# Optimization experiments

Hardware: AMD Instinct MI355X
Metric: run time of the kernel (lower is better)

Reference implementation:

```python
import jax, jax.numpy as jnp
import numpy as np

QUERY_DIM = 1024
KV_DIM = 768
NUM_HEADS = 16
HEAD_DIM = QUERY_DIM // NUM_HEADS


def setup_inputs() -> dict:
    key = jax.random.key(0)
    ks = jax.random.split(key, 11)
    B, Sq, Skv = 4, 2048, 2048
    s_q = 1.0 / np.sqrt(QUERY_DIM)
    s_kv = 1.0 / np.sqrt(KV_DIM)
    return {
        "query": jax.random.normal(ks[0], (B, Sq, QUERY_DIM), jnp.float32),
        "key": jax.random.normal(ks[1], (B, Skv, KV_DIM), jnp.float32),
        "value": jax.random.normal(ks[2], (B, Skv, KV_DIM), jnp.float32),
        "Wq": jax.random.uniform(ks[3], (QUERY_DIM, QUERY_DIM), jnp.float32, -s_q, s_q),
        "bq": jax.random.uniform(ks[4], (QUERY_DIM,), jnp.float32, -s_q, s_q),
        "Wk": jax.random.uniform(ks[5], (KV_DIM, QUERY_DIM), jnp.float32, -s_kv, s_kv),
        "bk": jax.random.uniform(ks[6], (QUERY_DIM,), jnp.float32, -s_kv, s_kv),
        "Wv": jax.random.uniform(ks[7], (KV_DIM, QUERY_DIM), jnp.float32, -s_kv, s_kv),
        "bv": jax.random.uniform(ks[8], (QUERY_DIM,), jnp.float32, -s_kv, s_kv),
        "Wo": jax.random.uniform(ks[9], (QUERY_DIM, QUERY_DIM), jnp.float32, -s_q, s_q),
        "bo": jax.random.uniform(ks[10], (QUERY_DIM,), jnp.float32, -s_q, s_q),
    }


def reference(query, key, value, Wq, bq, Wk, bk, Wv, bv, Wo, bo):
    B, Sq, _ = query.shape
    Skv = key.shape[1]
    H, D = NUM_HEADS, HEAD_DIM
    # linear projections, then split heads: [B, H, S, D]
    q = (query @ Wq + bq).reshape(B, Sq, H, D).transpose(0, 2, 1, 3)
    k = (key @ Wk + bk).reshape(B, Skv, H, D).transpose(0, 2, 1, 3)
    v = (value @ Wv + bv).reshape(B, Skv, H, D).transpose(0, 2, 1, 3)
    scores = jnp.einsum("bhqd,bhkd->bhqk", q, k) / np.sqrt(D).astype(jnp.float32)
    probs = jax.nn.softmax(scores, axis=-1)
    ctx = jnp.einsum("bhqk,bhkd->bhqd", probs, v)
    ctx = ctx.transpose(0, 2, 1, 3).reshape(B, Sq, H * D)
    return ctx @ Wo + bo
```

## Files before the change

### kernel.cpp

```cpp
#include <hip/hip_runtime.h>

typedef unsigned short u16;
typedef unsigned int u32;
typedef __attribute__((ext_vector_type(8))) short bf16x8;
typedef __attribute__((ext_vector_type(4))) float f32x4;

__device__ __forceinline__ u16 f2bf(float f) {
  union { float f; u32 u; } v; v.f = f;
  u32 r = v.u + 0x7fffu + ((v.u >> 16) & 1u);
  return (u16)(r >> 16);
}
__device__ __forceinline__ u16 f2bf_fast(float f) {
  union { float f; u32 u; } v; v.f = f;
  return (u16)((v.u + 0x8000u) >> 16);
}

__device__ __forceinline__ void gll16(const u16* g, u16* l) {
  __builtin_amdgcn_global_load_lds((__attribute__((address_space(1))) void*)(void*)g,
                                   (__attribute__((address_space(3))) void*)(void*)l,
                                   16, 0, 0);
}

__global__ void conv_bf16(const float* __restrict__ in, u16* __restrict__ out, int n) {
  int i = (blockIdx.x * 256 + threadIdx.x) * 4;
  if (i < n) {
    float4 v = *(const float4*)(in + i);
    ushort4 o;
    o.x = f2bf(v.x); o.y = f2bf(v.y); o.z = f2bf(v.z); o.w = f2bf(v.w);
    *(ushort4*)(out + i) = o;
  }
}

__global__ void transpose_bf16(const float* __restrict__ W, u16* __restrict__ T,
                               int K, int N) {
  __shared__ u16 tile[64 * 72];
  const int k0 = blockIdx.x * 64, n0 = blockIdx.y * 64;
  const int t = threadIdx.x, c = t & 63, rb = t >> 6;
#pragma unroll
  for (int rr = 0; rr < 64; rr += 4) {
    int r = rr + rb;
    tile[r * 72 + c] = f2bf(W[(size_t)(k0 + r) * N + n0 + c]);
  }
  __syncthreads();
#pragma unroll
  for (int rr = 0; rr < 64; rr += 4) {
    int n = rr + rb;
    T[(size_t)(n0 + n) * K + k0 + c] = tile[c * 72 + n];
  }
}

__global__ __launch_bounds__(256, 3) void gemm_bf16(
    const u16* __restrict__ A, const u16* __restrict__ Bt,
    const float* __restrict__ bias, u16* __restrict__ outb,
    float* __restrict__ outf, int K, int mode) {
  __shared__ __align__(16) u16 smem[18432];
  u16* lA = smem;
  u16* lB = smem + 128 * 64;
  const int tid = threadIdx.x;
  const int bm = blockIdx.x * 128;
  const int bn = blockIdx.y * 128;
  const int wid = tid >> 6, lane = tid & 63;
  const int wm = (wid >> 1) * 64, wn = (wid & 1) * 64;
  const int lrow = lane & 15, quad = lane >> 4;
  const int wrow = lane >> 3, wchk = lane & 7;
  const int sw = lrow & 7;
  f32x4 acc[4][4] = {};
  for (int k0 = 0; k0 < K; k0 += 64) {
    const u16* gA = A + (size_t)(bm + wid * 32) * K + k0;
    const u16* gB = Bt + (size_t)(bn + wid * 32) * K + k0;
#pragma unroll
    for (int c = 0; c < 4; c++) {
      gll16(gA + (size_t)(c * 8 + wrow) * K + (wchk ^ wrow) * 8, &lA[(wid * 32 + c * 8) * 64]);
      gll16(gB + (size_t)(c * 8 + wrow) * K + (wchk ^ wrow) * 8, &lB[(wid * 32 + c * 8) * 64]);
    }
    __syncthreads();
#pragma unroll
    for (int ks = 0; ks < 2; ks++) {
      bf16x8 af[4], bfr[4];
#pragma unroll
      for (int i = 0; i < 4; i++)
        af[i] = *(const bf16x8*)&lA[(wm + i * 16 + lrow) * 64 + ((ks * 4 + quad) ^ sw) * 8];
#pragma unroll
      for (int j = 0; j < 4; j++)
        bfr[j] = *(const bf16x8*)&lB[(wn + j * 16 + lrow) * 64 + ((ks * 4 + quad) ^ sw) * 8];
#pragma unroll
      for (int i = 0; i < 4; i++)
#pragma unroll
        for (int j = 0; j < 4; j++)
          acc[i][j] = __builtin_amdgcn_mfma_f32_16x16x32_bf16(af[i], bfr[j], acc[i][j], 0, 0, 0);
    }
    __syncthreads();
  }
  if (mode == 1) {
    u16* tile = smem + wid * (64 * 72);
#pragma unroll
    for (int i = 0; i < 4; i++)
#pragma unroll
      for (int j = 0; j < 4; j++)
#pragma unroll
        for (int r = 0; r < 4; r++) {
          int s_l = i * 16 + quad * 4 + r;
          int d_l = j * 16 + lrow;
          tile[d_l * 72 + s_l] = f2bf(acc[i][j][r] + bias[bn + wn + d_l]);
        }
    __syncthreads();
#pragma unroll
    for (int dd = 0; dd < 8; dd++) {
      int d_l = dd * 8 + (lane >> 3);
      int s_l = (lane & 7) * 8;
      bf16x8 vv = *(const bf16x8*)&tile[d_l * 72 + s_l];
      int row = bm + wm + s_l;
      int col = bn + wn + d_l;
      int b = row >> 11, s = row & 2047;
      int h = col >> 6, d = col & 63;
      *(bf16x8*)&outb[((size_t)(b * 16 + h) * 64 + d) * 2048 + s] = vv;
    }
    return;
  }
#pragma unroll
  for (int i = 0; i < 4; i++)
#pragma unroll
    for (int j = 0; j < 4; j++)
#pragma unroll
      for (int r = 0; r < 4; r++) {
        int row = bm + wm + i * 16 + quad * 4 + r;
        int col = bn + wn + j * 16 + lrow;
        float v = acc[i][j][r] + bias[col];
        if (mode == 2) {
          outf[(size_t)row * 1024 + col] = v;
        } else {
          int b = row >> 11, s = row & 2047;
          int h = col >> 6, d = col & 63;
          outb[((size_t)(b * 16 + h) * 2048 + s) * 64 + d] = f2bf(v);
        }
      }
}

__global__ __launch_bounds__(256, 3) void flash_attn(
    const u16* __restrict__ Q, const u16* __restrict__ Kt,
    const u16* __restrict__ Vt, u16* __restrict__ ctx) {
  __shared__ __align__(16) u16 lK[128 * 64];
  __shared__ __align__(16) u16 lV[64 * 128];
  __shared__ __align__(16) u16 lP[4][16 * 136];
  const int bh = blockIdx.x;
  const int q0 = blockIdx.y * 64;
  const int tid = threadIdx.x, wid = tid >> 6, lane = tid & 63;
  const int lrow = lane & 15, quad = lane >> 4;
  const int sw = lrow & 7;
  const size_t base = (size_t)bh * 2048 * 64;
  bf16x8 qf[2];
#pragma unroll
  for (int ks = 0; ks < 2; ks++)
    qf[ks] = *(const bf16x8*)(Q + base + (size_t)(q0 + wid * 16 + lrow) * 64 + ks * 32 + quad * 8);
  f32x4 of[4] = {};
  float lsum[4] = {0.f, 0.f, 0.f, 0.f};
  const int wrow8 = lane >> 3, wchk8 = lane & 7;
  const int wrow16 = lane >> 4, wchk16 = lane & 15;
  const float C = 0.18033688011112042f;
  for (int kv0 = 0; kv0 < 2048; kv0 += 128) {
    __syncthreads();
    const u16* gK = Kt + base + (size_t)(kv0 + wid * 32) * 64;
    const u16* gV = Vt + base + (size_t)(wid * 16) * 2048 + kv0;
#pragma unroll
    for (int c = 0; c < 4; c++) {
      gll16(gK + (size_t)(c * 8 + wrow8) * 64 + (wchk8 ^ wrow8) * 8,
            &lK[(wid * 32 + c * 8) * 64]);
      gll16(gV + (size_t)(c * 4 + wrow16) * 2048 + (wchk16 ^ (c * 4 + wrow16)) * 8,
            &lV[(wid * 16 + c * 4) * 128]);
    }
    __syncthreads();
    f32x4 sf[8];
#pragma unroll
    for (int n = 0; n < 8; n++) {
      bf16x8 k0f = *(const bf16x8*)&lK[(n * 16 + lrow) * 64 + (quad ^ sw) * 8];
      bf16x8 k1f = *(const bf16x8*)&lK[(n * 16 + lrow) * 64 + ((4 + quad) ^ sw) * 8];
      f32x4 s = {};
      s = __builtin_amdgcn_mfma_f32_16x16x32_bf16(qf[0], k0f, s, 0, 0, 0);
      s = __builtin_amdgcn_mfma_f32_16x16x32_bf16(qf[1], k1f, s, 0, 0, 0);
      sf[n] = s;
    }
#pragma unroll
    for (int n = 0; n < 8; n++)
#pragma unroll
      for (int r = 0; r < 4; r++) {
        float p = __builtin_amdgcn_exp2f(sf[n][r] * C);
        lsum[r] += p;
        lP[wid][(quad * 4 + r) * 136 + n * 16 + lrow] = f2bf_fast(p);
      }
    __syncthreads();
#pragma unroll
    for (int kstep = 0; kstep < 4; kstep++) {
      bf16x8 pf = *(const bf16x8*)&lP[wid][lrow * 136 + kstep * 32 + quad * 8];
#pragma unroll
      for (int n = 0; n < 4; n++) {
        bf16x8 vf = *(const bf16x8*)&lV[(n * 16 + lrow) * 128 + ((kstep * 4 + quad) ^ lrow) * 8];
        of[n] = __builtin_amdgcn_mfma_f32_16x16x32_bf16(pf, vf, of[n], 0, 0, 0);
      }
    }
  }
#pragma unroll
  for (int r = 0; r < 4; r++) {
#pragma unroll
    for (int off = 1; off < 16; off <<= 1) lsum[r] += __shfl_xor(lsum[r], off, 64);
  }
  const int b = bh >> 4, h = bh & 15;
#pragma unroll
  for (int r = 0; r < 4; r++) {
    float inv = 1.f / lsum[r];
#pragma unroll
    for (int n = 0; n < 4; n++) {
      int row = q0 + wid * 16 + quad * 4 + r;
      int col = h * 64 + n * 16 + lrow;
      ctx[((size_t)b * 2048 + row) * 1024 + col] = f2bf(of[n][r] * inv);
    }
  }
}

extern "C" void kernel_launch(void* const* d_in, const int* in_sizes, int n_in,
                              void* d_out, int out_size, void* d_ws, size_t ws_size,
                              hipStream_t stream) {
  const float* query = (const float*)d_in[0];
  const float* key   = (const float*)d_in[1];
  const float* value = (const float*)d_in[2];
  const float* Wq = (const float*)d_in[3];
  const float* bq = (const float*)d_in[4];
  const float* Wk = (const float*)d_in[5];
  const float* bk = (const float*)d_in[6];
  const float* Wv = (const float*)d_in[7];
  const float* bv = (const float*)d_in[8];
  const float* Wo = (const float*)d_in[9];
  const float* bo = (const float*)d_in[10];
  float* out = (float*)d_out;
  char* ws = (char*)d_ws;

  const size_t SZ_QKV = (size_t)8192 * 1024 * 2;
  const size_t SZ_KIN = (size_t)8192 * 768 * 2;
  u16* q_ws  = (u16*)(ws);
  u16* k_ws  = (u16*)(ws + SZ_QKV);
  u16* vt_ws = (u16*)(ws + 2 * SZ_QKV);
  u16* qin   = (u16*)(ws + 3 * SZ_QKV);
  u16* kin   = (u16*)(ws + 4 * SZ_QKV);
  u16* vin   = (u16*)(ws + 4 * SZ_QKV + SZ_KIN);
  u16* ctx   = qin;
  u16* wq_t  = (u16*)(ws + 4 * SZ_QKV + 2 * SZ_KIN);
  u16* wk_t  = wq_t + 1024 * 1024;
  u16* wv_t  = wk_t + 1024 * 768;
  u16* wo_t  = wv_t + 1024 * 768;

  conv_bf16<<<8192, 256, 0, stream>>>(query, qin, 8388608);
  conv_bf16<<<6144, 256, 0, stream>>>(key, kin, 6291456);
  conv_bf16<<<6144, 256, 0, stream>>>(value, vin, 6291456);
  transpose_bf16<<<dim3(16, 16), 256, 0, stream>>>(Wq, wq_t, 1024, 1024);
  transpose_bf16<<<dim3(12, 16), 256, 0, stream>>>(Wk, wk_t, 768, 1024);
  transpose_bf16<<<dim3(12, 16), 256, 0, stream>>>(Wv, wv_t, 768, 1024);
  transpose_bf16<<<dim3(16, 16), 256, 0, stream>>>(Wo, wo_t, 1024, 1024);

  gemm_bf16<<<dim3(64, 8), 256, 0, stream>>>(qin, wq_t, bq, q_ws, nullptr, 1024, 0);
  gemm_bf16<<<dim3(64, 8), 256, 0, stream>>>(kin, wk_t, bk, k_ws, nullptr, 768, 0);
  gemm_bf16<<<dim3(64, 8), 256, 0, stream>>>(vin, wv_t, bv, vt_ws, nullptr, 768, 1);

  flash_attn<<<dim3(64, 32), 256, 0, stream>>>(q_ws, k_ws, vt_ws, ctx);

  gemm_bf16<<<dim3(64, 8), 256, 0, stream>>>(ctx, wo_t, bo, nullptr, out, 1024, 2);
}
```

Baseline: 363.6 us.

## Split flash attention KV tile across waves instead of query rows

Each wave now computes scores for all 64 query rows against its own 32-key slice of the 128-key tile, using transposed MFMAs (K as the A operand). P values are packed two per word, written to a per-wave LDS buffer and read back with only an lgkmcnt wait instead of a block barrier. Partial outputs and row sums are reduced across waves through LDS at the end, with vectorized bf16 stores. The intent is to cut redundant K/V LDS reads and the mid-loop barrier, at the cost of 4x more accumulator registers (64 floats of output per lane), which may hurt occupancy under launch_bounds(256,3), plus a serialized final reduction.

```diff
diff --git a/kernel.cpp b/kernel.cpp
--- a/kernel.cpp
+++ b/kernel.cpp
@@ -2,6 +2,7 @@
 
 typedef unsigned short u16;
 typedef unsigned int u32;
+typedef unsigned long long u64;
 typedef __attribute__((ext_vector_type(8))) short bf16x8;
 typedef __attribute__((ext_vector_type(4))) float f32x4;
 
@@ -10,9 +11,9 @@
   u32 r = v.u + 0x7fffu + ((v.u >> 16) & 1u);
   return (u16)(r >> 16);
 }
-__device__ __forceinline__ u16 f2bf_fast(float f) {
-  union { float f; u32 u; } v; v.f = f;
-  return (u16)((v.u + 0x8000u) >> 16);
+__device__ __forceinline__ u32 pack2bf(float a, float b) {
+  union { float f; u32 u; } x, y; x.f = a; y.f = b;
+  return ((y.u + 0x8000u) & 0xffff0000u) | ((x.u + 0x8000u) >> 16);
 }
 
 __device__ __forceinline__ void gll16(const u16* g, u16* l) {
@@ -139,21 +140,24 @@
 __global__ __launch_bounds__(256, 3) void flash_attn(
     const u16* __restrict__ Q, const u16* __restrict__ Kt,
     const u16* __restrict__ Vt, u16* __restrict__ ctx) {
-  __shared__ __align__(16) u16 lK[128 * 64];
-  __shared__ __align__(16) u16 lV[64 * 128];
-  __shared__ __align__(16) u16 lP[4][16 * 136];
+  __shared__ __align__(16) u16 smem[26624];
+  u16* lK = smem;
+  u16* lV = smem + 8192;
+  const int tid = threadIdx.x, wid = tid >> 6, lane = tid & 63;
+  u16* lP = smem + 16384 + wid * 2560;
   const int bh = blockIdx.x;
   const int q0 = blockIdx.y * 64;
-  const int tid = threadIdx.x, wid = tid >> 6, lane = tid & 63;
   const int lrow = lane & 15, quad = lane >> 4;
   const int sw = lrow & 7;
   const size_t base = (size_t)bh * 2048 * 64;
-  bf16x8 qf[2];
-#pragma unroll
-  for (int ks = 0; ks < 2; ks++)
-    qf[ks] = *(const bf16x8*)(Q + base + (size_t)(q0 + wid * 16 + lrow) * 64 + ks * 32 + quad * 8);
-  f32x4 of[4] = {};
-  float lsum[4] = {0.f, 0.f, 0.f, 0.f};
+  bf16x8 qf[4][2];
+#pragma unroll
+  for (int qt = 0; qt < 4; qt++)
+#pragma unroll
+    for (int ks = 0; ks < 2; ks++)
+      qf[qt][ks] = *(const bf16x8*)(Q + base + (size_t)(q0 + qt * 16 + lrow) * 64 + ks * 32 + quad * 8);
+  f32x4 of[4][4] = {};
+  float lsumq[4] = {0.f, 0.f, 0.f, 0.f};
   const int wrow8 = lane >> 3, wchk8 = lane & 7;
   const int wrow16 = lane >> 4, wchk16 = lane & 15;
   const float C = 0.18033688011112042f;
@@ -169,50 +173,83 @@
             &lV[(wid * 16 + c * 4) * 128]);
     }
     __syncthreads();
-    f32x4 sf[8];
-#pragma unroll
-    for (int n = 0; n < 8; n++) {
-      bf16x8 k0f = *(const bf16x8*)&lK[(n * 16 + lrow) * 64 + (quad ^ sw) * 8];
-      bf16x8 k1f = *(const bf16x8*)&lK[(n * 16 + lrow) * 64 + ((4 + quad) ^ sw) * 8];
-      f32x4 s = {};
-      s = __builtin_amdgcn_mfma_f32_16x16x32_bf16(qf[0], k0f, s, 0, 0, 0);
-      s = __builtin_amdgcn_mfma_f32_16x16x32_bf16(qf[1], k1f, s, 0, 0, 0);
-      sf[n] = s;
-    }
-#pragma unroll
-    for (int n = 0; n < 8; n++)
-#pragma unroll
-      for (int r = 0; r < 4; r++) {
-        float p = __builtin_amdgcn_exp2f(sf[n][r] * C);
-        lsum[r] += p;
-        lP[wid][(quad * 4 + r) * 136 + n * 16 + lrow] = f2bf_fast(p);
+    f32x4 sfT[2][4];
+#pragma unroll
+    for (int nt = 0; nt < 2; nt++) {
+      bf16x8 kf0 = *(const bf16x8*)&lK[((wid * 2 + nt) * 16 + lrow) * 64 + (quad ^ sw) * 8];
+      bf16x8 kf1 = *(const bf16x8*)&lK[((wid * 2 + nt) * 16 + lrow) * 64 + ((4 + quad) ^ sw) * 8];
+#pragma unroll
+      for (int qt = 0; qt < 4; qt++) {
+        f32x4 s = {};
+        s = __builtin_amdgcn_mfma_f32_16x16x32_bf16(kf0, qf[qt][0], s, 0, 0, 0);
+        s = __builtin_amdgcn_mfma_f32_16x16x32_bf16(kf1, qf[qt][1], s, 0, 0, 0);
+        sfT[nt][qt] = s;
       }
-    __syncthreads();
-#pragma unroll
-    for (int kstep = 0; kstep < 4; kstep++) {
-      bf16x8 pf = *(const bf16x8*)&lP[wid][lrow * 136 + kstep * 32 + quad * 8];
-#pragma unroll
-      for (int n = 0; n < 4; n++) {
-        bf16x8 vf = *(const bf16x8*)&lV[(n * 16 + lrow) * 128 + ((kstep * 4 + quad) ^ lrow) * 8];
-        of[n] = __builtin_amdgcn_mfma_f32_16x16x32_bf16(pf, vf, of[n], 0, 0, 0);
+    }
+#pragma unroll
+    for (int nt = 0; nt < 2; nt++)
+#pragma unroll
+      for (int qt = 0; qt < 4; qt++) {
+        float p0 = __builtin_amdgcn_exp2f(sfT[nt][qt][0] * C);
+        float p1 = __builtin_amdgcn_exp2f(sfT[nt][qt][1] * C);
+        float p2 = __builtin_amdgcn_exp2f(sfT[nt][qt][2] * C);
+        float p3 = __builtin_amdgcn_exp2f(sfT[nt][qt][3] * C);
+        lsumq[qt] += (p0 + p1) + (p2 + p3);
+        u64 pk = ((u64)pack2bf(p2, p3) << 32) | pack2bf(p0, p1);
+        *(u64*)&lP[(qt * 16 + lrow) * 40 + nt * 16 + quad * 4] = pk;
       }
-    }
-  }
-#pragma unroll
-  for (int r = 0; r < 4; r++) {
-#pragma unroll
-    for (int off = 1; off < 16; off <<= 1) lsum[r] += __shfl_xor(lsum[r], off, 64);
+    __asm__ volatile("s_waitcnt lgkmcnt(0)" ::: "memory");
+#pragma unroll
+    for (int qt = 0; qt < 4; qt++) {
+      bf16x8 pf = *(const bf16x8*)&lP[(qt * 16 + lrow) * 40 + quad * 8];
+#pragma unroll
+      for (int dt = 0; dt < 4; dt++) {
+        bf16x8 vf = *(const bf16x8*)&lV[(dt * 16 + lrow) * 128 + ((wid * 4 + quad) ^ lrow) * 8];
+        of[qt][dt] = __builtin_amdgcn_mfma_f32_16x16x32_bf16(pf, vf, of[qt][dt], 0, 0, 0);
+      }
+    }
+  }
+  float lsw[4];
+#pragma unroll
+  for (int qt = 0; qt < 4; qt++) {
+    float v = lsumq[qt];
+    v += __shfl_xor(v, 16, 64);
+    v += __shfl_xor(v, 32, 64);
+    lsw[qt] = v;
+  }
+  __syncthreads();
+  float* lsums = (float*)(smem + 16384);
+  if (quad == 0) {
+#pragma unroll
+    for (int qt = 0; qt < 4; qt++) lsums[wid * 64 + qt * 16 + lrow] = lsw[qt];
+  }
+  float* rbuf = (float*)smem;
+  for (int w = 0; w < 4; w++) {
+    if (wid == w) {
+#pragma unroll
+      for (int qt = 0; qt < 4; qt++)
+#pragma unroll
+        for (int dt = 0; dt < 4; dt++)
+#pragma unroll
+          for (int r = 0; r < 4; r++) {
+            int q = qt * 16 + quad * 4 + r;
+            int d = dt * 16 + lrow;
+            if (w == 0) rbuf[q * 66 + d] = of[qt][dt][r];
+            else        rbuf[q * 66 + d] += of[qt][dt][r];
+          }
+    }
+    __syncthreads();
   }
   const int b = bh >> 4, h = bh & 15;
 #pragma unroll
-  for (int r = 0; r < 4; r++) {
-    float inv = 1.f / lsum[r];
-#pragma unroll
-    for (int n = 0; n < 4; n++) {
-      int row = q0 + wid * 16 + quad * 4 + r;
-      int col = h * 64 + n * 16 + lrow;
-      ctx[((size_t)b * 2048 + row) * 1024 + col] = f2bf(of[n][r] * inv);
-    }
+  for (int it = 0; it < 2; it++) {
+    int q = wid * 16 + it * 8 + (lane >> 3);
+    int d0 = (lane & 7) * 8;
+    float inv = 1.f / (lsums[q] + lsums[64 + q] + lsums[128 + q] + lsums[192 + q]);
+    u16 o[8];
+#pragma unroll
+    for (int j = 0; j < 8; j++) o[j] = f2bf(rbuf[q * 66 + d0 + j] * inv);
+    *(bf16x8*)&ctx[((size_t)b * 2048 + q0 + q) * 1024 + h * 64 + d0] = *(bf16x8*)o;
   }
 }
 
```

New measurement: 354.9 us. 2.4% less time.
